# Optimization experiments

Measured on AMD Instinct MI355X. Metric: run time of the kernel, lower is better.

Reference implementation:

```python
import jax, jax.numpy as jnp
import numpy as np

N_BLOCKS = 96
N = N_BLOCKS ** 2          # number of image blocks = n_blocks^2
D = 1024                   # feature dim (fixed by Linear(1024+1, 128))
EPS_COS = 1e-6             # eps of F.cosine_similarity
EPS_BN = 1e-5              # BatchNorm1d eps


def setup_inputs() -> dict:
    key = jax.random.key(0)
    ks = jax.random.split(key, 6)
    return {
        "features": jax.random.normal(ks[0], (N, D), dtype=jnp.float32),
        "scores": jax.random.uniform(ks[1], (N,), dtype=jnp.float32),
        "W1": jax.random.normal(ks[2], (D + 1, 128), dtype=jnp.float32) * 0.03,
        "b1": jnp.zeros((128,), jnp.float32),
        "g1": jnp.ones((128,), jnp.float32),
        "be1": jnp.zeros((128,), jnp.float32),
        "W2": jax.random.normal(ks[3], (128, 64), dtype=jnp.float32) * 0.08,
        "b2": jnp.zeros((64,), jnp.float32),
        "g2": jnp.ones((64,), jnp.float32),
        "be2": jnp.zeros((64,), jnp.float32),
        "W3": jax.random.normal(ks[4], (64, 1), dtype=jnp.float32) * 0.12,
        "b3": jnp.zeros((1,), jnp.float32),
    }


def _gaussian_similarity(features):
    # Vectorized form of the O(N^2) pairwise loop:
    #   cos_ij = <f_i, f_j> / max(|f_i||f_j|, eps)
    #   sigma^2 = D * (0.5 + 0.5 * cos)  ->  2*sigma^2 = D * (1 + cos)
    #   sim_ij = exp(-|f_i - f_j|^2 / (2*sigma^2)),  sim_ii = 1
    sq = jnp.sum(features * features, axis=-1)          # [N] squared norms
    gram = features @ features.T                          # [N, N] big GEMM
    norms = jnp.sqrt(sq)
    cos = gram / jnp.maximum(norms[:, None] * norms[None, :], EPS_COS)
    d2 = jnp.maximum(sq[:, None] + sq[None, :] - 2.0 * gram, 0.0)
    denom = jnp.maximum(jnp.float32(D) * (1.0 + cos), EPS_COS)
    sim = jnp.exp(-d2 / denom)
    eye = jnp.eye(sim.shape[0], dtype=bool)
    return jnp.where(eye, jnp.float32(1.0), sim)


def _bn_eval(h, gamma, beta):
    # BatchNorm1d in eval mode with init running stats (mean=0, var=1).
    return gamma * (h / jnp.sqrt(1.0 + EPS_BN)) + beta


def reference(features, scores, W1, b1, g1, be1, W2, b2, g2, be2, W3, b3):
    sim = _gaussian_similarity(features)                  # [N, N]
    x = jnp.concatenate([features, scores[:, None]], axis=1)  # [N, D+1]
    h = jax.nn.relu(_bn_eval(x @ W1 + b1, g1, be1))       # [N, 128]
    h = jax.nn.relu(_bn_eval(h @ W2 + b2, g2, be2))       # [N, 64]
    agg = jax.nn.sigmoid(h @ W3 + b3)[:, 0]               # [N]
    sim_mean = jnp.mean(sim, axis=1)                      # [N]
    # Torch broadcast [N,1] * [N] -> [N,N], then .mean() == mean(agg)*mean(sim_mean)
    return jnp.mean(agg) * jnp.mean(sim_mean)


if __name__ == "__main__":
    out = reference(**setup_inputs())
    print(out)
```

## Files before the change

kernel.cpp:

```cpp
#include <hip/hip_runtime.h>

#define N_IMG 9216
#define DFEAT 1024
#define NBR 72
#define NPAIR 1332

typedef __attribute__((ext_vector_type(8))) short short8;
typedef __attribute__((ext_vector_type(4))) float floatx4;
typedef __attribute__((ext_vector_type(16))) float floatx16;
typedef __attribute__((ext_vector_type(4))) int intx4;
typedef __attribute__((ext_vector_type(8))) int intx8;

#define C1F 0.0014088818759657845f
#define C2F 0.05308355472172724f

__device__ __forceinline__ void async_copy16(const void* g, void* l) {
  __builtin_amdgcn_global_load_lds((const __attribute__((address_space(1))) void*)g,
                                   (__attribute__((address_space(3))) void*)l,
                                   16, 0, 0);
}

__device__ __forceinline__ unsigned short f2bf(float x) {
  union { float f; unsigned u; } a; a.f = x;
  unsigned u = a.u;
  u += 0x7fffu + ((u >> 16) & 1u);
  return (unsigned short)(u >> 16);
}

__device__ __forceinline__ unsigned q4(float z) {
  unsigned sg = (__float_as_uint(z) >> 28) & 8u;
  float a = fabsf(z);
  unsigned c = (a < 0.25f) ? 0u : (a < 0.75f) ? 1u : (a < 1.25f) ? 2u :
               (a < 1.75f) ? 3u : (a < 2.5f)  ? 4u : (a < 3.5f)  ? 5u :
               (a < 5.0f)  ? 6u : 7u;
  return c | sg;
}
__device__ __forceinline__ unsigned short pk4(float4 v, float sc) {
  unsigned b0 = q4(v.x * sc) | (q4(v.y * sc) << 4);
  unsigned b1 = q4(v.z * sc) | (q4(v.w * sc) << 4);
  return (unsigned short)(b0 | (b1 << 8));
}

__device__ __forceinline__ intx8 ext8(intx4 v) {
  intx8 r;
  r[0] = v[0]; r[1] = v[1]; r[2] = v[2]; r[3] = v[3];
  r[4] = 0; r[5] = 0; r[6] = 0; r[7] = 0;
  return r;
}

__global__ __launch_bounds__(256) void convert_prep(const float* __restrict__ f,
                                                    const float* __restrict__ W1,
                                                    unsigned char* __restrict__ fbT,
                                                    float* __restrict__ sL,
                                                    float* __restrict__ pL,
                                                    unsigned short* __restrict__ W1t,
                                                    double* __restrict__ sums) {
  int b = blockIdx.x, t = threadIdx.x;
  if (b < 2304) {
    int lane = t & 63, wave = t >> 6;
    int row = b * 4 + wave;
    const float4* src = (const float4*)f + (size_t)row * 256;
    float4 v0 = src[lane], v1 = src[64 + lane], v2 = src[128 + lane], v3 = src[192 + lane];
    float s = v0.x * v0.x + v0.y * v0.y + v0.z * v0.z + v0.w * v0.w
            + v1.x * v1.x + v1.y * v1.y + v1.z * v1.z + v1.w * v1.w
            + v2.x * v2.x + v2.y * v2.y + v2.z * v2.z + v2.w * v2.w
            + v3.x * v3.x + v3.y * v3.y + v3.z * v3.z + v3.w * v3.w;
#pragma unroll
    for (int off = 32; off > 0; off >>= 1) s += __shfl_xor(s, off, 64);
    float zsc = rsqrtf(s) * 32.f;
    unsigned short u0 = pk4(v0, zsc), u1 = pk4(v1, zsc),
                   u2 = pk4(v2, zsc), u3 = pk4(v3, zsc);
    unsigned char* tb = fbT + (size_t)(row >> 5) * 16384 + (row & 31) * 32 + (lane & 15) * 2;
    int ko = (lane >> 4) * 1024;
    *(unsigned short*)(tb + ko) = u0;
    *(unsigned short*)(tb + ko + 4096) = u1;
    *(unsigned short*)(tb + ko + 8192) = u2;
    *(unsigned short*)(tb + ko + 12288) = u3;
    if (lane == 0) {
      sL[row] = s * C1F;
      pL[row] = sqrtf(s) * C2F;
    }
  } else {
    int j = b - 2304;
    if (j == 0 && t < 2) sums[t] = 0.0;
    for (int k = t; k < DFEAT; k += 256)
      W1t[(size_t)j * DFEAT + k] = f2bf(W1[(size_t)k * 128 + j]);
  }
}

__global__ __launch_bounds__(256, 2) void gram_sim(const unsigned char* __restrict__ fbT,
                                                   const float* __restrict__ sL,
                                                   const float* __restrict__ pL,
                                                   double* __restrict__ sums) {
  int x = blockIdx.x & 7, ii = blockIdx.x >> 3;
  int L = (x < 4) ? x * 167 + ii : 668 + (x - 4) * 166 + ii;
  int rem = L, bcol = 0;
  for (;;) {
    int mlim = 2 * bcol + 2; if (mlim > NBR) mlim = NBR;
    if (rem < mlim) break;
    rem -= mlim; bcol++;
  }
  int brow = rem;

  __shared__ float sA[128], pA[128], sB[256], pB[256];
  __shared__ float wpart[4];

  int t = threadIdx.x, lane = t & 63, wave = t >> 6;
  if (t < 128) { sA[t] = sL[brow * 128 + t]; pA[t] = pL[brow * 128 + t]; }
  sB[t] = sL[bcol * 256 + t];
  pB[t] = pL[bcol * 256 + t];
  __syncthreads();

  const int wr = (wave & 1) * 64, wc = (wave >> 1) * 128;
  const int r32 = lane & 31, kh = lane >> 5;
  const int loff = r32 * 32 + kh * 16;

  const unsigned char* pa0 = fbT + (size_t)(brow * 4 + (wr >> 5)) * 16384 + loff;
  const unsigned char* pa1 = pa0 + 16384;
  const unsigned char* pb0 = fbT + (size_t)(bcol * 8 + (wc >> 5)) * 16384 + loff;
  const unsigned char* pb1 = pb0 + 16384;
  const unsigned char* pb2 = pb0 + 32768;
  const unsigned char* pb3 = pb0 + 49152;

  floatx16 acc[2][4];
#pragma unroll
  for (int mi = 0; mi < 2; mi++)
#pragma unroll
    for (int ni = 0; ni < 4; ni++)
#pragma unroll
      for (int e = 0; e < 16; e++) acc[mi][ni][e] = 0.f;

  intx4 bA[3][2], bB[3][4];
#define LDSET(s, kb)                                                        \
  {                                                                         \
    const int o = (kb) * 1024;                                              \
    bA[s][0] = *(const intx4*)(pa0 + o); bA[s][1] = *(const intx4*)(pa1 + o); \
    bB[s][0] = *(const intx4*)(pb0 + o); bB[s][1] = *(const intx4*)(pb1 + o); \
    bB[s][2] = *(const intx4*)(pb2 + o); bB[s][3] = *(const intx4*)(pb3 + o); \
  }
  LDSET(0, 0)
  LDSET(1, 1)
#pragma unroll
  for (int kb = 0; kb < 16; kb++) {
    const int cur = kb % 3, nxt = (kb + 2) % 3;
    if (kb < 14) LDSET(nxt, kb + 2)
    intx8 A8[2], B8[4];
#pragma unroll
    for (int mi = 0; mi < 2; mi++) A8[mi] = ext8(bA[cur][mi]);
#pragma unroll
    for (int ni = 0; ni < 4; ni++) B8[ni] = ext8(bB[cur][ni]);
#pragma unroll
    for (int mi = 0; mi < 2; mi++)
#pragma unroll
      for (int ni = 0; ni < 4; ni++)
        acc[mi][ni] = __builtin_amdgcn_mfma_scale_f32_32x32x64_f8f6f4(
            A8[mi], B8[ni], acc[mi][ni], 4, 4,
            0, 0x7F7F7F7F, 0, 0x7F7F7F7F);
  }
#undef LDSET

  const bool interior = (brow < 2 * bcol);
  float lsum = 0.f;
#pragma unroll
  for (int ni = 0; ni < 4; ni++) {
    int j_loc = wc + ni * 32 + r32;
    float sj = sB[j_loc], pj = pB[j_loc];
    int j_g = bcol * 256 + j_loc;
#pragma unroll
    for (int mi = 0; mi < 2; mi++) {
      int rbase = wr + mi * 32 + 4 * kh;
#pragma unroll
      for (int reg = 0; reg < 16; reg++) {
        int i_loc = rbase + (reg & 3) + 8 * (reg >> 2);
        float g = acc[mi][ni][reg];
        float si = sA[i_loc], pi = pA[i_loc];
        float r = __builtin_amdgcn_rcpf(1024.f + g);
        float del = pi * pj;
        float gam = si + sj + del;
        float tt = gam * r;
        float sim = __builtin_amdgcn_exp2f(fmaf(-1024.f, tt, del));
        if (interior) {
          lsum += sim;
        } else {
          int i_g = brow * 128 + i_loc;
          lsum += (i_g < j_g) ? 2.f * sim : (i_g == j_g ? 1.f : 0.f);
        }
      }
    }
  }
  if (interior) lsum *= 2.f;
#pragma unroll
  for (int off = 32; off > 0; off >>= 1) lsum += __shfl_down(lsum, off, 64);
  if (lane == 0) wpart[wave] = lsum;
  __syncthreads();
  if (t == 0)
    atomicAdd(&sums[0], (double)(wpart[0] + wpart[1] + wpart[2] + wpart[3]));
}

__global__ __launch_bounds__(256) void mlp_full(const float* __restrict__ f,
                                                const unsigned short* __restrict__ W1t,
                                                const float* __restrict__ scores,
                                                const float* __restrict__ W1,
                                                const float* __restrict__ b1,
                                                const float* __restrict__ g1,
                                                const float* __restrict__ be1,
                                                const float* __restrict__ W2, const float* __restrict__ b2,
                                                const float* __restrict__ g2, const float* __restrict__ be2,
                                                const float* __restrict__ W3, const float* __restrict__ b3,
                                                double* __restrict__ sums) {
  int r0 = blockIdx.x * 32;

  __shared__ __align__(16) float As32[32 * 64];
  __shared__ __align__(16) unsigned short Bs[128 * 64];
  __shared__ float h1s[32][128];
  __shared__ float h2s[32][65];
  __shared__ float sc[32], b1s[128], g1s[128], be1s[128], wls[128], ls[32];

  int t = threadIdx.x, lane = t & 63, wave = t >> 6;
  if (t < 32) sc[t] = scores[r0 + t];
  if (t < 128) {
    b1s[t] = b1[t]; g1s[t] = g1[t]; be1s[t] = be1[t];
    wls[t] = W1[(size_t)DFEAT * 128 + t];
  }

  floatx4 acc[4];
#pragma unroll
  for (int b = 0; b < 4; b++) acc[b] = (floatx4){0.f, 0.f, 0.f, 0.f};

  const int wr = (wave & 1) * 16, wc = (wave >> 1) * 64;

  for (int k0 = 0; k0 < DFEAT; k0 += 64) {
    __syncthreads();
    {
      int c = t, rA = c >> 4, p = c & 15, l = p ^ (rA & 15);
      async_copy16(f + (size_t)(r0 + rA) * DFEAT + k0 + l * 4, (char*)As32 + c * 16);
      c = t + 256; rA = c >> 4; p = c & 15; l = p ^ (rA & 15);
      async_copy16(f + (size_t)(r0 + rA) * DFEAT + k0 + l * 4, (char*)As32 + c * 16);
#pragma unroll
      for (int q = 0; q < 4; q++) {
        int cc = t + q * 256, rB = cc >> 3, pp = cc & 7, ll = pp ^ (rB & 7);
        async_copy16(W1t + (size_t)rB * DFEAT + k0 + ll * 8, (char*)Bs + cc * 16);
      }
    }
    __syncthreads();

    const int mrow = lane & 15;
#pragma unroll
    for (int ks = 0; ks < 2; ks++) {
      const int kq = ks * 32 + (lane >> 4) * 8;
      short8 a, b[4];
      {
        int row = wr + mrow;
        int l0 = kq >> 2;
        int p0 = l0 ^ (row & 15), p1 = (l0 + 1) ^ (row & 15);
        float4 f0 = *(const float4*)&As32[row * 64 + p0 * 4];
        float4 f1 = *(const float4*)&As32[row * 64 + p1 * 4];
        a[0] = (short)f2bf(f0.x); a[1] = (short)f2bf(f0.y);
        a[2] = (short)f2bf(f0.z); a[3] = (short)f2bf(f0.w);
        a[4] = (short)f2bf(f1.x); a[5] = (short)f2bf(f1.y);
        a[6] = (short)f2bf(f1.z); a[7] = (short)f2bf(f1.w);
      }
#pragma unroll
      for (int nt = 0; nt < 4; nt++) {
        int row = wc + nt * 16 + mrow;
        int p = (kq >> 3) ^ (row & 7);
        b[nt] = *(const short8*)&Bs[row * 64 + p * 8];
      }
#pragma unroll
      for (int nt = 0; nt < 4; nt++)
        acc[nt] = __builtin_amdgcn_mfma_f32_16x16x32_bf16(a, b[nt], acc[nt], 0, 0, 0);
    }
  }

  const float inv = 1.0f / sqrtf(1.0f + 1e-5f);
  const int rq = (lane >> 4) * 4, cn = lane & 15;
#pragma unroll
  for (int nt = 0; nt < 4; nt++) {
    int j = wc + nt * 16 + cn;
    float bj = b1s[j], gj = g1s[j] * inv, bej = be1s[j], wj = wls[j];
#pragma unroll
    for (int rr = 0; rr < 4; rr++) {
      int iL = wr + rq + rr;
      float pre = acc[nt][rr] + sc[iL] * wj + bj;
      h1s[iL][j] = fmaxf(gj * pre + bej, 0.f);
    }
  }
  __syncthreads();

  {
    int j = t & 63, rg = (t >> 6) * 8;
    float a2[8];
#pragma unroll
    for (int rr = 0; rr < 8; rr++) a2[rr] = 0.f;
    for (int k = 0; k < 128; k++) {
      float w = W2[k * 64 + j];
#pragma unroll
      for (int rr = 0; rr < 8; rr++) a2[rr] = fmaf(h1s[rg + rr][k], w, a2[rr]);
    }
    float scv = g2[j] * inv, bi = b2[j], be = be2[j];
#pragma unroll
    for (int rr = 0; rr < 8; rr++)
      h2s[rg + rr][j] = fmaxf(scv * (a2[rr] + bi) + be, 0.f);
  }
  __syncthreads();

  if (t < 32) {
    float z = b3[0];
#pragma unroll
    for (int k = 0; k < 64; k++) z = fmaf(h2s[t][k], W3[k], z);
    ls[t] = 1.f / (1.f + __expf(-z));
  }
  __syncthreads();
  if (t == 0) {
    float s = 0.f;
#pragma unroll
    for (int iL = 0; iL < 32; iL++) s += ls[iL];
    atomicAdd(&sums[1], (double)s);
  }
}

__global__ void finalize(const double* __restrict__ sums, float* __restrict__ out) {
  double simmean = sums[0] / ((double)N_IMG * (double)N_IMG);
  double aggmean = sums[1] / (double)N_IMG;
  out[0] = (float)(aggmean * simmean);
}

extern "C" void kernel_launch(void* const* d_in, const int* in_sizes, int n_in,
                              void* d_out, int out_size, void* d_ws, size_t ws_size,
                              hipStream_t stream) {
  const float* f      = (const float*)d_in[0];
  const float* scores = (const float*)d_in[1];
  const float* W1 = (const float*)d_in[2];
  const float* b1 = (const float*)d_in[3];
  const float* g1 = (const float*)d_in[4];
  const float* be1 = (const float*)d_in[5];
  const float* W2 = (const float*)d_in[6];
  const float* b2 = (const float*)d_in[7];
  const float* g2 = (const float*)d_in[8];
  const float* be2 = (const float*)d_in[9];
  const float* W3 = (const float*)d_in[10];
  const float* b3 = (const float*)d_in[11];

  char* ws = (char*)d_ws;
  unsigned char* fbT  = (unsigned char*)ws;
  float* sL           = (float*)(ws + 4718592);
  float* pL           = (float*)(ws + 4755456);
  unsigned short* W1t = (unsigned short*)(ws + 4792320);
  double* sums        = (double*)(ws + 5054464);

  convert_prep<<<2432, 256, 0, stream>>>(f, W1, fbT, sL, pL, W1t, sums);
  gram_sim<<<NPAIR, 256, 0, stream>>>(fbT, sL, pL, sums);
  mlp_full<<<288, 256, 0, stream>>>(f, W1t, scores, W1, b1, g1, be1,
                                    W2, b2, g2, be2, W3, b3, sums);
  finalize<<<1, 1, 0, stream>>>(sums, (float*)d_out);
}
```

Baseline: 181.3 us.

## Use square 128x128 gram tiles with a new FP4 layout and fused finalize

Switches the gram kernel from 128x256 triangular tiles to 128x128 upper-triangle tiles, raising the block count and occupancy hint to three blocks per CU. The packed FP4 feature layout is changed so each lane reads one contiguous 16-byte chunk, and the triple-buffered register prefetch is replaced by a simple per-iteration load. The finalize kernel is folded into the MLP kernel through an atomic completion counter, removing one launch. Smaller tiles mean more redundant loads per FLOP, and dropping the prefetch may expose memory latency.

```diff
diff --git a/kernel.cpp b/kernel.cpp
--- a/kernel.cpp
+++ b/kernel.cpp
@@ -3,7 +3,7 @@
 #define N_IMG 9216
 #define DFEAT 1024
 #define NBR 72
-#define NPAIR 1332
+#define NPAIR 2628
 
 typedef __attribute__((ext_vector_type(8))) short short8;
 typedef __attribute__((ext_vector_type(4))) float floatx4;
@@ -41,20 +41,14 @@
   return (unsigned short)(b0 | (b1 << 8));
 }
 
-__device__ __forceinline__ intx8 ext8(intx4 v) {
-  intx8 r;
-  r[0] = v[0]; r[1] = v[1]; r[2] = v[2]; r[3] = v[3];
-  r[4] = 0; r[5] = 0; r[6] = 0; r[7] = 0;
-  return r;
-}
-
 __global__ __launch_bounds__(256) void convert_prep(const float* __restrict__ f,
                                                     const float* __restrict__ W1,
                                                     unsigned char* __restrict__ fbT,
                                                     float* __restrict__ sL,
                                                     float* __restrict__ pL,
                                                     unsigned short* __restrict__ W1t,
-                                                    double* __restrict__ sums) {
+                                                    double* __restrict__ sums,
+                                                    unsigned* __restrict__ cnt) {
   int b = blockIdx.x, t = threadIdx.x;
   if (b < 2304) {
     int lane = t & 63, wave = t >> 6;
@@ -70,12 +64,13 @@
     float zsc = rsqrtf(s) * 32.f;
     unsigned short u0 = pk4(v0, zsc), u1 = pk4(v1, zsc),
                    u2 = pk4(v2, zsc), u3 = pk4(v3, zsc);
-    unsigned char* tb = fbT + (size_t)(row >> 5) * 16384 + (row & 31) * 32 + (lane & 15) * 2;
-    int ko = (lane >> 4) * 1024;
-    *(unsigned short*)(tb + ko) = u0;
-    *(unsigned short*)(tb + ko + 4096) = u1;
-    *(unsigned short*)(tb + ko + 8192) = u2;
-    *(unsigned short*)(tb + ko + 12288) = u3;
+    unsigned char* tb = fbT + (size_t)(row >> 5) * 16384 + ((lane >> 3) & 1) * 512
+                      + (row & 31) * 16 + (lane & 7) * 2;
+    int kbase = (lane >> 4) * 1024;
+    *(unsigned short*)(tb + kbase) = u0;
+    *(unsigned short*)(tb + kbase + 4096) = u1;
+    *(unsigned short*)(tb + kbase + 8192) = u2;
+    *(unsigned short*)(tb + kbase + 12288) = u3;
     if (lane == 0) {
       sL[row] = s * C1F;
       pL[row] = sqrtf(s) * C2F;
@@ -83,89 +78,75 @@
   } else {
     int j = b - 2304;
     if (j == 0 && t < 2) sums[t] = 0.0;
+    if (j == 0 && t == 2) *cnt = 0u;
     for (int k = t; k < DFEAT; k += 256)
       W1t[(size_t)j * DFEAT + k] = f2bf(W1[(size_t)k * 128 + j]);
   }
 }
 
-__global__ __launch_bounds__(256, 2) void gram_sim(const unsigned char* __restrict__ fbT,
+__global__ __launch_bounds__(256, 3) void gram_sim(const unsigned char* __restrict__ fbT,
                                                    const float* __restrict__ sL,
                                                    const float* __restrict__ pL,
                                                    double* __restrict__ sums) {
   int x = blockIdx.x & 7, ii = blockIdx.x >> 3;
-  int L = (x < 4) ? x * 167 + ii : 668 + (x - 4) * 166 + ii;
+  int L = (x < 4) ? x * 329 + ii : 1316 + (x - 4) * 328 + ii;
   int rem = L, bcol = 0;
   for (;;) {
-    int mlim = 2 * bcol + 2; if (mlim > NBR) mlim = NBR;
-    if (rem < mlim) break;
-    rem -= mlim; bcol++;
+    if (rem < bcol + 1) break;
+    rem -= bcol + 1; bcol++;
   }
   int brow = rem;
 
-  __shared__ float sA[128], pA[128], sB[256], pB[256];
+  __shared__ float sA[128], pA[128], sB[128], pB[128];
   __shared__ float wpart[4];
 
   int t = threadIdx.x, lane = t & 63, wave = t >> 6;
   if (t < 128) { sA[t] = sL[brow * 128 + t]; pA[t] = pL[brow * 128 + t]; }
-  sB[t] = sL[bcol * 256 + t];
-  pB[t] = pL[bcol * 256 + t];
-  __syncthreads();
-
-  const int wr = (wave & 1) * 64, wc = (wave >> 1) * 128;
+  else { sB[t - 128] = sL[bcol * 128 + (t - 128)]; pB[t - 128] = pL[bcol * 128 + (t - 128)]; }
+  __syncthreads();
+
+  const int wr = (wave & 1) * 64, wc = (wave >> 1) * 64;
   const int r32 = lane & 31, kh = lane >> 5;
-  const int loff = r32 * 32 + kh * 16;
-
-  const unsigned char* pa0 = fbT + (size_t)(brow * 4 + (wr >> 5)) * 16384 + loff;
-  const unsigned char* pa1 = pa0 + 16384;
-  const unsigned char* pb0 = fbT + (size_t)(bcol * 8 + (wc >> 5)) * 16384 + loff;
-  const unsigned char* pb1 = pb0 + 16384;
-  const unsigned char* pb2 = pb0 + 32768;
-  const unsigned char* pb3 = pb0 + 49152;
-
-  floatx16 acc[2][4];
+
+  const unsigned char* a0 = fbT + (size_t)(brow * 4 + (wr >> 5)) * 16384 + lane * 16;
+  const unsigned char* a1 = a0 + 16384;
+  const unsigned char* b0 = fbT + (size_t)(bcol * 4 + (wc >> 5)) * 16384 + lane * 16;
+  const unsigned char* b1 = b0 + 16384;
+
+  floatx16 acc[2][2];
 #pragma unroll
   for (int mi = 0; mi < 2; mi++)
 #pragma unroll
-    for (int ni = 0; ni < 4; ni++)
+    for (int ni = 0; ni < 2; ni++)
 #pragma unroll
       for (int e = 0; e < 16; e++) acc[mi][ni][e] = 0.f;
 
-  intx4 bA[3][2], bB[3][4];
-#define LDSET(s, kb)                                                        \
-  {                                                                         \
-    const int o = (kb) * 1024;                                              \
-    bA[s][0] = *(const intx4*)(pa0 + o); bA[s][1] = *(const intx4*)(pa1 + o); \
-    bB[s][0] = *(const intx4*)(pb0 + o); bB[s][1] = *(const intx4*)(pb1 + o); \
-    bB[s][2] = *(const intx4*)(pb2 + o); bB[s][3] = *(const intx4*)(pb3 + o); \
-  }
-  LDSET(0, 0)
-  LDSET(1, 1)
+  intx8 A0 = {0,0,0,0,0,0,0,0}, A1 = {0,0,0,0,0,0,0,0};
+  intx8 B0 = {0,0,0,0,0,0,0,0}, B1 = {0,0,0,0,0,0,0,0};
+
 #pragma unroll
   for (int kb = 0; kb < 16; kb++) {
-    const int cur = kb % 3, nxt = (kb + 2) % 3;
-    if (kb < 14) LDSET(nxt, kb + 2)
-    intx8 A8[2], B8[4];
-#pragma unroll
-    for (int mi = 0; mi < 2; mi++) A8[mi] = ext8(bA[cur][mi]);
-#pragma unroll
-    for (int ni = 0; ni < 4; ni++) B8[ni] = ext8(bB[cur][ni]);
-#pragma unroll
-    for (int mi = 0; mi < 2; mi++)
-#pragma unroll
-      for (int ni = 0; ni < 4; ni++)
-        acc[mi][ni] = __builtin_amdgcn_mfma_scale_f32_32x32x64_f8f6f4(
-            A8[mi], B8[ni], acc[mi][ni], 4, 4,
-            0, 0x7F7F7F7F, 0, 0x7F7F7F7F);
-  }
-#undef LDSET
-
-  const bool interior = (brow < 2 * bcol);
+    const int o = kb * 1024;
+    *(intx4*)&A0 = *(const intx4*)(a0 + o);
+    *(intx4*)&A1 = *(const intx4*)(a1 + o);
+    *(intx4*)&B0 = *(const intx4*)(b0 + o);
+    *(intx4*)&B1 = *(const intx4*)(b1 + o);
+    acc[0][0] = __builtin_amdgcn_mfma_scale_f32_32x32x64_f8f6f4(
+        A0, B0, acc[0][0], 4, 4, 0, 0x7F7F7F7F, 0, 0x7F7F7F7F);
+    acc[0][1] = __builtin_amdgcn_mfma_scale_f32_32x32x64_f8f6f4(
+        A0, B1, acc[0][1], 4, 4, 0, 0x7F7F7F7F, 0, 0x7F7F7F7F);
+    acc[1][0] = __builtin_amdgcn_mfma_scale_f32_32x32x64_f8f6f4(
+        A1, B0, acc[1][0], 4, 4, 0, 0x7F7F7F7F, 0, 0x7F7F7F7F);
+    acc[1][1] = __builtin_amdgcn_mfma_scale_f32_32x32x64_f8f6f4(
+        A1, B1, acc[1][1], 4, 4, 0, 0x7F7F7F7F, 0, 0x7F7F7F7F);
+  }
+
+  const bool interior = (brow < bcol);
   float lsum = 0.f;
 #pragma unroll
-  for (int ni = 0; ni < 4; ni++) {
+  for (int ni = 0; ni < 2; ni++) {
     int j_loc = wc + ni * 32 + r32;
     float sj = sB[j_loc], pj = pB[j_loc];
-    int j_g = bcol * 256 + j_loc;
 #pragma unroll
     for (int mi = 0; mi < 2; mi++) {
       int rbase = wr + mi * 32 + 4 * kh;
@@ -182,8 +163,7 @@
         if (interior) {
           lsum += sim;
         } else {
-          int i_g = brow * 128 + i_loc;
-          lsum += (i_g < j_g) ? 2.f * sim : (i_g == j_g ? 1.f : 0.f);
+          lsum += (i_loc < j_loc) ? 2.f * sim : (i_loc == j_loc ? 1.f : 0.f);
         }
       }
     }
@@ -207,7 +187,9 @@
                                                 const float* __restrict__ W2, const float* __restrict__ b2,
                                                 const float* __restrict__ g2, const float* __restrict__ be2,
                                                 const float* __restrict__ W3, const float* __restrict__ b3,
-                                                double* __restrict__ sums) {
+                                                double* __restrict__ sums,
+                                                unsigned* __restrict__ cnt,
+                                                float* __restrict__ out) {
   int r0 = blockIdx.x * 32;
 
   __shared__ __align__(16) float As32[32 * 64];
@@ -316,13 +298,14 @@
 #pragma unroll
     for (int iL = 0; iL < 32; iL++) s += ls[iL];
     atomicAdd(&sums[1], (double)s);
-  }
-}
-
-__global__ void finalize(const double* __restrict__ sums, float* __restrict__ out) {
-  double simmean = sums[0] / ((double)N_IMG * (double)N_IMG);
-  double aggmean = sums[1] / (double)N_IMG;
-  out[0] = (float)(aggmean * simmean);
+    __threadfence();
+    unsigned c = atomicAdd(cnt, 1u);
+    if (c == 287u) {
+      double simmean = sums[0] / ((double)N_IMG * (double)N_IMG);
+      double aggmean = sums[1] / (double)N_IMG;
+      out[0] = (float)(aggmean * simmean);
+    }
+  }
 }
 
 extern "C" void kernel_launch(void* const* d_in, const int* in_sizes, int n_in,
@@ -347,10 +330,10 @@
   float* pL           = (float*)(ws + 4755456);
   unsigned short* W1t = (unsigned short*)(ws + 4792320);
   double* sums        = (double*)(ws + 5054464);
-
-  convert_prep<<<2432, 256, 0, stream>>>(f, W1, fbT, sL, pL, W1t, sums);
+  unsigned* cnt       = (unsigned*)(ws + 5054480);
+
+  convert_prep<<<2432, 256, 0, stream>>>(f, W1, fbT, sL, pL, W1t, sums, cnt);
   gram_sim<<<NPAIR, 256, 0, stream>>>(fbT, sL, pL, sums);
   mlp_full<<<288, 256, 0, stream>>>(f, W1t, scores, W1, b1, g1, be1,
-                                    W2, b2, g2, be2, W3, b3, sums);
-  finalize<<<1, 1, 0, stream>>>(sums, (float*)d_out);
-}
+                                    W2, b2, g2, be2, W3, b3, sums, cnt, (float*)d_out);
+}
```

After: 186.4 us. +2.8%, slower.
